# Performance work log

Measured on AMD Instinct MI355X. Metric: run time of the kernel, lower is better.

## Reference

```python
import jax, jax.numpy as jnp
import numpy as np

VOCAB, NUM_CLASSES, E, H = 50257, 20, 64, 64
B, T = 128, 2048


def setup_inputs() -> dict:
    key = jax.random.key(0)
    ks = jax.random.split(key, 16)
    s_ih = 1.0 / np.sqrt(H)
    u = lambda k, shape: jax.random.uniform(k, shape, jnp.float32, -s_ih, s_ih)
    return {
        'tokens': jax.random.randint(ks[0], (B, T), 0, VOCAB),
        'emb': jax.random.normal(ks[1], (VOCAB, E), jnp.float32),
        # forward-direction GRU params (PyTorch layout: [3H, *], gate order r,z,n)
        'wih_f': u(ks[2], (3 * H, E)), 'whh_f': u(ks[3], (3 * H, H)),
        'bih_f': u(ks[4], (3 * H,)), 'bhh_f': u(ks[5], (3 * H,)),
        # backward-direction GRU params
        'wih_b': u(ks[6], (3 * H, E)), 'whh_b': u(ks[7], (3 * H, H)),
        'bih_b': u(ks[8], (3 * H,)), 'bhh_b': u(ks[9], (3 * H,)),
        # classifier: Linear(4H -> H), GELU, Linear(H -> C)
        'w1': u(ks[10], (H, 4 * H)), 'b1': u(ks[11], (H,)),
        'w2': u(ks[12], (NUM_CLASSES, H)), 'b2': u(ks[13], (NUM_CLASSES,)),
    }


def _gru_dir(x, wih, whh, bih, bhh):
    # x: [B, T, E] -> outputs [B, T, H]; PyTorch GRU gate math, gates (r, z, n)
    xg = jnp.einsum('bte,ge->tbg', x, wih) + bih  # precompute input projections [T,B,3H]
    h0 = jnp.zeros((x.shape[0], H), x.dtype)

    def step(h, xg_t):
        hg = h @ whh.T + bhh
        xr, xz, xn = jnp.split(xg_t, 3, axis=-1)
        hr, hz, hn = jnp.split(hg, 3, axis=-1)
        r = jax.nn.sigmoid(xr + hr)
        z = jax.nn.sigmoid(xz + hz)
        n = jnp.tanh(xn + r * hn)
        h_new = (1.0 - z) * n + z * h
        return h_new, h_new

    _, hs = jax.lax.scan(step, h0, xg)  # hs: [T, B, H]
    return hs.transpose(1, 0, 2)


def reference(tokens, emb, wih_f, whh_f, bih_f, bhh_f,
              wih_b, whh_b, bih_b, bhh_b, w1, b1, w2, b2):
    x = emb[tokens]  # [B, T, E]
    h_fwd = _gru_dir(x, wih_f, whh_f, bih_f, bhh_f)
    h_bwd = _gru_dir(x[:, ::-1], wih_b, whh_b, bih_b, bhh_b)[:, ::-1]
    encoded = jnp.concatenate([h_fwd, h_bwd], axis=-1)  # [B, T, 2H]
    feats = jnp.concatenate([encoded.mean(axis=1), encoded.max(axis=1)], axis=-1)  # [B, 4H]
    hid = jax.nn.gelu(feats @ w1.T + b1, approximate=False)
    return hid @ w2.T + b2  # [B, C]
```

## Files before the change

### kernel.cpp

```cpp
#include <hip/hip_runtime.h>
#include <hip/hip_bf16.h>
#include <math.h>

#define VOCAB 50257
#define NCLS 20
#define EDIM 64
#define HDIM 64
#define BATCH 128
#define TLEN 2048

typedef float v2f __attribute__((ext_vector_type(2)));

__device__ float g_P[(size_t)2 * VOCAB * 192];
__device__ float g_feats[BATCH * 256];

__device__ __forceinline__ float fast_rcp(float x) { return __builtin_amdgcn_rcpf(x); }

__device__ __forceinline__ float fsigmoid(float x) {
    return fast_rcp(1.f + __expf(-x));
}
__device__ __forceinline__ float ftanh(float x) {
    float e = __expf(2.f * x);
    return 1.f - 2.f * fast_rcp(e + 1.f);
}

__global__ __launch_bounds__(384) void precompute_P(
    const float* __restrict__ emb,
    const float* __restrict__ wih_f, const float* __restrict__ bih_f,
    const float* __restrict__ wih_b, const float* __restrict__ bih_b)
{
    const int t = threadIdx.x;
    const int dir = t / 192;
    const int g = t % 192;
    const float* wih = dir ? wih_b : wih_f;
    const float* bih = dir ? bih_b : bih_f;

    float w[64];
#pragma unroll
    for (int e = 0; e < 64; e += 4) {
        float4 v = *(const float4*)(wih + (size_t)g * 64 + e);
        w[e] = v.x; w[e + 1] = v.y; w[e + 2] = v.z; w[e + 3] = v.w;
    }
    const float bias = bih[g];
    float* Pd = g_P + (size_t)dir * VOCAB * 192;

    for (int v = blockIdx.x * 2; v < VOCAB; v += gridDim.x * 2) {
        const int v1ok = (v + 1 < VOCAB);
        const float4* e0 = (const float4*)(emb + (size_t)v * 64);
        const float4* e1 = (const float4*)(emb + (size_t)(v1ok ? v + 1 : v) * 64);
        float a0 = bias, a1 = bias;
#pragma unroll
        for (int e4 = 0; e4 < 16; e4++) {
            float4 x = e0[e4];
            float4 y = e1[e4];
            a0 = fmaf(x.x, w[4 * e4 + 0], a0);
            a1 = fmaf(y.x, w[4 * e4 + 0], a1);
            a0 = fmaf(x.y, w[4 * e4 + 1], a0);
            a1 = fmaf(y.y, w[4 * e4 + 1], a1);
            a0 = fmaf(x.z, w[4 * e4 + 2], a0);
            a1 = fmaf(y.z, w[4 * e4 + 2], a1);
            a0 = fmaf(x.w, w[4 * e4 + 3], a0);
            a1 = fmaf(y.w, w[4 * e4 + 3], a1);
        }
        Pd[(size_t)v * 192 + g] = a0;
        if (v1ok) Pd[(size_t)(v + 1) * 192 + g] = a1;
    }
}

__global__ __launch_bounds__(64, 1) void gru_seq(
    const int* __restrict__ tokens,
    const float* __restrict__ whh_f, const float* __restrict__ bhh_f,
    const float* __restrict__ whh_b, const float* __restrict__ bhh_b)
{
    const int lane = threadIdx.x;
    const int blk = blockIdx.x;
    const int b = blk >> 1;
    const int dir = blk & 1;
    const float* whh = dir ? whh_b : whh_f;
    const float* bhh = dir ? bhh_b : bhh_f;
    const float* Pd = g_P + (size_t)dir * VOCAB * 192;

    __shared__ __align__(16) float h_lds[64];
    __shared__ __align__(16) int tok_lds[TLEN];

    {
        const int4* src = (const int4*)(tokens + (size_t)b * TLEN);
        int4* dst = (int4*)tok_lds;
        for (int t = lane; t < TLEN / 4; t += 64) dst[t] = src[t];
    }

    v2f wr[32], wz[32], wn[32];
    {
        const float* pr = whh + (size_t)(0 + lane) * 64;
        const float* pz = whh + (size_t)(64 + lane) * 64;
        const float* pn = whh + (size_t)(128 + lane) * 64;
#pragma unroll
        for (int k = 0; k < 16; k++) {
            float4 a = *(const float4*)(pr + 4 * k);
            wr[2 * k] = (v2f){a.x, a.y}; wr[2 * k + 1] = (v2f){a.z, a.w};
            float4 c = *(const float4*)(pz + 4 * k);
            wz[2 * k] = (v2f){c.x, c.y}; wz[2 * k + 1] = (v2f){c.z, c.w};
            float4 d = *(const float4*)(pn + 4 * k);
            wn[2 * k] = (v2f){d.x, d.y}; wn[2 * k + 1] = (v2f){d.z, d.w};
        }
    }
    const float br = bhh[lane], bz = bhh[64 + lane], bn = bhh[128 + lane];

    h_lds[lane] = 0.f;
    float h = 0.f, sum = 0.f, mx = -INFINITY;

    auto tok_at = [&](int s) -> int {
        int ss = s < TLEN ? s : TLEN - 1;
        return tok_lds[dir ? (TLEN - 1 - ss) : ss];
    };

    float xr[4], xz[4], xn[4];
#pragma unroll
    for (int d = 0; d < 4; d++) {
        const float* rd = Pd + (size_t)tok_at(d) * 192;
        xr[d] = rd[lane]; xz[d] = rd[64 + lane]; xn[d] = rd[128 + lane];
    }
    int tokN = tok_at(4);

#pragma unroll 4
    for (int s = 0; s < TLEN; s++) {
        const int slot = s & 3;

        const float* rp = Pd + (size_t)tokN * 192;
        float pxr = rp[lane], pxz = rp[64 + lane], pxn = rp[128 + lane];
        tokN = tok_at(s + 5);

        v2f ar0 = {0.f, 0.f}, ar1 = {0.f, 0.f};
        v2f az0 = {0.f, 0.f}, az1 = {0.f, 0.f};
        v2f an0 = {0.f, 0.f}, an1 = {0.f, 0.f};
#pragma unroll
        for (int k = 0; k < 16; k++) {
            float4 h4 = *(const float4*)(h_lds + 4 * k);
            v2f h01 = {h4.x, h4.y}, h23 = {h4.z, h4.w};
            ar0 = __builtin_elementwise_fma(h01, wr[2 * k], ar0);
            az0 = __builtin_elementwise_fma(h01, wz[2 * k], az0);
            an0 = __builtin_elementwise_fma(h01, wn[2 * k], an0);
            ar1 = __builtin_elementwise_fma(h23, wr[2 * k + 1], ar1);
            az1 = __builtin_elementwise_fma(h23, wz[2 * k + 1], az1);
            an1 = __builtin_elementwise_fma(h23, wn[2 * k + 1], an1);
        }
        float hr = (ar0.x + ar0.y) + (ar1.x + ar1.y);
        float hz = (az0.x + az0.y) + (az1.x + az1.y);
        float hn = (an0.x + an0.y) + (an1.x + an1.y);

        float r = fsigmoid(xr[slot] + hr + br);
        float z = fsigmoid(xz[slot] + hz + bz);
        float n = ftanh(xn[slot] + r * (hn + bn));
        h = fmaf(z, h - n, n);
        sum += h;
        mx = fmaxf(mx, h);

        h_lds[lane] = h;

        xr[slot] = pxr; xz[slot] = pxz; xn[slot] = pxn;
    }

    g_feats[b * 256 + dir * 64 + lane] = sum * (1.f / TLEN);
    g_feats[b * 256 + 128 + dir * 64 + lane] = mx;
}

__global__ __launch_bounds__(64) void classifier(
    const float* __restrict__ w1, const float* __restrict__ b1,
    const float* __restrict__ w2, const float* __restrict__ b2,
    float* __restrict__ out)
{
    const int b = blockIdx.x;
    const int i = threadIdx.x;
    __shared__ float f[256];
    __shared__ float hid[64];
    for (int c = i; c < 256; c += 64) f[c] = g_feats[b * 256 + c];
    __syncthreads();

    float acc = b1[i];
    const float* wrow = w1 + (size_t)i * 256;
#pragma unroll 16
    for (int c = 0; c < 256; c++) acc = fmaf(f[c], wrow[c], acc);
    hid[i] = acc * 0.5f * (1.f + erff(acc * 0.70710678118654752f));
    __syncthreads();

    if (i < NCLS) {
        float o = b2[i];
        const float* w2r = w2 + (size_t)i * 64;
#pragma unroll
        for (int j = 0; j < 64; j++) o = fmaf(hid[j], w2r[j], o);
        out[b * NCLS + i] = o;
    }
}

extern "C" void kernel_launch(void* const* d_in, const int* in_sizes, int n_in,
                              void* d_out, int out_size, void* d_ws, size_t ws_size,
                              hipStream_t stream) {
    const int*   tokens = (const int*)  d_in[0];
    const float* emb    = (const float*)d_in[1];
    const float* wih_f  = (const float*)d_in[2];
    const float* whh_f  = (const float*)d_in[3];
    const float* bih_f  = (const float*)d_in[4];
    const float* bhh_f  = (const float*)d_in[5];
    const float* wih_b  = (const float*)d_in[6];
    const float* whh_b  = (const float*)d_in[7];
    const float* bih_b  = (const float*)d_in[8];
    const float* bhh_b  = (const float*)d_in[9];
    const float* w1     = (const float*)d_in[10];
    const float* b1     = (const float*)d_in[11];
    const float* w2     = (const float*)d_in[12];
    const float* b2     = (const float*)d_in[13];
    float* out = (float*)d_out;

    precompute_P<<<1024, 384, 0, stream>>>(emb, wih_f, bih_f, wih_b, bih_b);
    gru_seq<<<2 * BATCH, 64, 0, stream>>>(tokens, whh_f, bhh_f, whh_b, bhh_b);
    classifier<<<BATCH, 64, 0, stream>>>(w1, b1, w2, b2, out);
}
```

Before: 977.9 us.

## Deepen GRU input prefetch to 8 steps with inline-asm loads and explicit waitcnt

```diff
diff --git a/kernel.cpp b/kernel.cpp
--- a/kernel.cpp
+++ b/kernel.cpp
@@ -114,54 +114,69 @@
         return tok_lds[dir ? (TLEN - 1 - ss) : ss];
     };
 
-    float xr[4], xz[4], xn[4];
-#pragma unroll
-    for (int d = 0; d < 4; d++) {
-        const float* rd = Pd + (size_t)tok_at(d) * 192;
-        xr[d] = rd[lane]; xz[d] = rd[64 + lane]; xn[d] = rd[128 + lane];
-    }
-    int tokN = tok_at(4);
-
-#pragma unroll 4
-    for (int s = 0; s < TLEN; s++) {
-        const int slot = s & 3;
-
-        const float* rp = Pd + (size_t)tokN * 192;
-        float pxr = rp[lane], pxz = rp[64 + lane], pxn = rp[128 + lane];
-        tokN = tok_at(s + 5);
-
-        v2f ar0 = {0.f, 0.f}, ar1 = {0.f, 0.f};
-        v2f az0 = {0.f, 0.f}, az1 = {0.f, 0.f};
-        v2f an0 = {0.f, 0.f}, an1 = {0.f, 0.f};
-#pragma unroll
-        for (int k = 0; k < 16; k++) {
-            float4 h4 = *(const float4*)(h_lds + 4 * k);
-            v2f h01 = {h4.x, h4.y}, h23 = {h4.z, h4.w};
-            ar0 = __builtin_elementwise_fma(h01, wr[2 * k], ar0);
-            az0 = __builtin_elementwise_fma(h01, wz[2 * k], az0);
-            an0 = __builtin_elementwise_fma(h01, wn[2 * k], an0);
-            ar1 = __builtin_elementwise_fma(h23, wr[2 * k + 1], ar1);
-            az1 = __builtin_elementwise_fma(h23, wz[2 * k + 1], az1);
-            an1 = __builtin_elementwise_fma(h23, wn[2 * k + 1], an1);
-        }
-        float hr = (ar0.x + ar0.y) + (ar1.x + ar1.y);
-        float hz = (az0.x + az0.y) + (az1.x + az1.y);
-        float hn = (an0.x + an0.y) + (an1.x + an1.y);
-
-        float r = fsigmoid(xr[slot] + hr + br);
-        float z = fsigmoid(xz[slot] + hz + bz);
-        float n = ftanh(xn[slot] + r * (hn + bn));
-        h = fmaf(z, h - n, n);
-        sum += h;
-        mx = fmaxf(mx, h);
-
-        h_lds[lane] = h;
-
-        xr[slot] = pxr; xz[slot] = pxz; xn[slot] = pxn;
-    }
+    float xr0, xz0, xn0, xr1, xz1, xn1, xr2, xz2, xn2, xr3, xz3, xn3;
+    float xr4, xz4, xn4, xr5, xz5, xn5, xr6, xz6, xn6, xr7, xz7, xn7;
+
+#define GRU_PRE(SL, D) do {                                                        \
+        const float* rd_ = Pd + (size_t)tok_at(D) * 192;                           \
+        asm volatile("global_load_dword %0, %1, off" : "=v"(xr##SL) : "v"(rd_ + lane));       \
+        asm volatile("global_load_dword %0, %1, off" : "=v"(xz##SL) : "v"(rd_ + 64 + lane));  \
+        asm volatile("global_load_dword %0, %1, off" : "=v"(xn##SL) : "v"(rd_ + 128 + lane)); \
+    } while (0)
+
+    GRU_PRE(0, 0); GRU_PRE(1, 1); GRU_PRE(2, 2); GRU_PRE(3, 3);
+    GRU_PRE(4, 4); GRU_PRE(5, 5); GRU_PRE(6, 6); GRU_PRE(7, 7);
+
+#define GRU_STEP(SL, SB) do {                                                      \
+        const int tN_ = tok_at((SB) + 8);                                          \
+        v2f ar0 = {0.f, 0.f}, ar1 = {0.f, 0.f};                                    \
+        v2f az0 = {0.f, 0.f}, az1 = {0.f, 0.f};                                    \
+        v2f an0 = {0.f, 0.f}, an1 = {0.f, 0.f};                                    \
+        _Pragma("unroll")                                                          \
+        for (int k = 0; k < 16; k++) {                                             \
+            float4 h4 = *(const float4*)(h_lds + 4 * k);                           \
+            v2f h01 = {h4.x, h4.y}, h23 = {h4.z, h4.w};                            \
+            ar0 = __builtin_elementwise_fma(h01, wr[2 * k], ar0);                  \
+            az0 = __builtin_elementwise_fma(h01, wz[2 * k], az0);                  \
+            an0 = __builtin_elementwise_fma(h01, wn[2 * k], an0);                  \
+            ar1 = __builtin_elementwise_fma(h23, wr[2 * k + 1], ar1);              \
+            az1 = __builtin_elementwise_fma(h23, wz[2 * k + 1], az1);              \
+            an1 = __builtin_elementwise_fma(h23, wn[2 * k + 1], an1);              \
+        }                                                                          \
+        float hr = (ar0.x + ar0.y) + (ar1.x + ar1.y);                              \
+        float hz = (az0.x + az0.y) + (az1.x + az1.y);                              \
+        float hn = (an0.x + an0.y) + (an1.x + an1.y);                              \
+        asm volatile("s_waitcnt vmcnt(21)" ::: "memory");                          \
+        __builtin_amdgcn_sched_barrier(0);                                         \
+        float r_ = fsigmoid(xr##SL + hr + br);                                     \
+        float z_ = fsigmoid(xz##SL + hz + bz);                                     \
+        float n_ = ftanh(xn##SL + r_ * (hn + bn));                                 \
+        h = fmaf(z_, h - n_, n_);                               \
+        sum += h;                                                                  \
+        mx = fmaxf(mx, h);                                                         \
+        h_lds[lane] = h;              \
+        const float* rp_ = Pd + (size_t)tN_ * 192;                                 \
+        asm volatile("global_load_dword %0, %1, off" : "=v"(xr##SL) : "v"(rp_ + lane));       \
+        asm volatile("global_load_dword %0, %1, off" : "=v"(xz##SL) : "v"(rp_ + 64 + lane));  \
+        asm volatile("global_load_dword %0, %1, off" : "=v"(xn##SL) : "v"(rp_ + 128 + lane)); \
+    } while (0)
+
+    for (int s = 0; s < TLEN; s += 8) {
+        GRU_STEP(0, s + 0);
+        GRU_STEP(1, s + 1);
+        GRU_STEP(2, s + 2);
+        GRU_STEP(3, s + 3);
+        GRU_STEP(4, s + 4);
+        GRU_STEP(5, s + 5);
+        GRU_STEP(6, s + 6);
+        GRU_STEP(7, s + 7);
+    }
+    asm volatile("s_waitcnt vmcnt(0)" ::: "memory");
 
     g_feats[b * 256 + dir * 64 + lane] = sum * (1.f / TLEN);
     g_feats[b * 256 + 128 + dir * 64 + lane] = mx;
+#undef GRU_PRE
+#undef GRU_STEP
 }
 
 __global__ __launch_bounds__(64) void classifier(
@@ -211,7 +226,7 @@
     const float* b2     = (const float*)d_in[13];
     float* out = (float*)d_out;
 
-    precompute_P<<<1024, 384, 0, stream>>>(emb, wih_f, bih_f, wih_b, bih_b);
+    precompute_P<<<4096, 384, 0, stream>>>(emb, wih_f, bih_f, wih_b, bih_b);
     gru_seq<<<2 * BATCH, 64, 0, stream>>>(tokens, whh_f, bhh_f, whh_b, bhh_b);
     classifier<<<BATCH, 64, 0, stream>>>(w1, b1, w2, b2, out);
 }
```

Result: slower. 1.398 ms (+43.0%).
